# Optimization experiments

Hardware: AMD Instinct MI355X
Metric: run time of the kernel (lower is better)

The kernel has to match this reference:

```python
import jax, jax.numpy as jnp
import numpy as np

D_MODEL = 1024; D_STATE = 128; HEADDIM = 64; D_CONV = 4; CHUNK = 256
D_INNER = 2 * D_MODEL; NHEADS = D_INNER // HEADDIM
CONV_DIM = D_INNER + 2 * D_STATE
D_IN_PROJ = 2 * D_INNER + 2 * D_STATE + NHEADS
POOL_SIZE = 50; SUMMARY_DIM = 64; TAU1 = 0.5; TAU2 = 0.3
RET_HEAD_DIM = SUMMARY_DIM // 4  # CrossTokenRetrieval n_heads=4
SCORER_HID = int(D_MODEL * 0.25)
B_SZ = 2; T_LEN = 1024
EPS = 1e-5


def _rmsnorm(x, w):
    var = jnp.mean(jnp.square(x), axis=-1, keepdims=True)
    return x * jax.lax.rsqrt(var + EPS) * w


def _ssd(xd, dA, Bm, Cm):
    # Mamba2 SSD chunked scan. xd=(b,T,h,p)=x*dt, dA=(b,T,h)=dt*A, Bm/Cm=(b,T,n)
    b, T, h, p = xd.shape
    c = T // CHUNK; l = CHUNK
    xd = xd.reshape(b, c, l, h, p)
    dA = dA.reshape(b, c, l, h).transpose(0, 3, 1, 2)           # (b,h,c,l)
    Bm = Bm.reshape(b, c, l, -1); Cm = Cm.reshape(b, c, l, -1)  # (b,c,l,n)
    cs = jnp.cumsum(dA, axis=-1)                                # (b,h,c,l)
    mask = jnp.tril(jnp.ones((l, l), bool))
    seg = jnp.where(mask, cs[..., :, None] - cs[..., None, :], -jnp.inf)
    L = jnp.exp(seg)                                            # (b,h,c,l,s)
    y_diag = jnp.einsum('bcln,bcsn,bhcls,bcshp->bclhp', Cm, Bm, L, xd)
    decay_states = jnp.exp(cs[..., -1:] - cs)                   # (b,h,c,l)
    states = jnp.einsum('bcln,bhcl,bclhp->bchpn', Bm, decay_states, xd)
    chunk_sum = jnp.pad(cs[..., -1], ((0, 0), (0, 0), (1, 0)))  # (b,h,c+1)
    cs2 = jnp.cumsum(chunk_sum, axis=-1)
    maskc = jnp.tril(jnp.ones((c + 1, c + 1), bool))
    segc = jnp.where(maskc, cs2[..., :, None] - cs2[..., None, :], -jnp.inf)
    decay_chunk = jnp.exp(segc)                                 # (b,h,c+1,c+1)
    states = jnp.concatenate([jnp.zeros_like(states[:, :1]), states], axis=1)
    prev = jnp.einsum('bhzc,bchpn->bzhpn', decay_chunk, states)[:, :-1]
    y_off = jnp.einsum('bcln,bchpn,bhcl->bclhp', Cm, prev, jnp.exp(cs))
    return (y_diag + y_off).reshape(b, T, h, p)


def _forward(x, norm_w, in_proj_w, conv_w, conv_b, dt_bias, A_log, D, ssm_norm_w,
             out_proj_w, scorer_w1, scorer_w2, summ_w, q_w, k_w, v_w, gate_w):
    b, T, _ = x.shape
    residual = x
    xn = _rmsnorm(x, norm_w)
    # --- Mamba2 ---
    zxbcdt = xn @ in_proj_w                                     # (b,T,4384)
    z = zxbcdt[..., :D_INNER]
    xBC = zxbcdt[..., D_INNER:D_INNER + CONV_DIM]
    dt = jax.nn.softplus(zxbcdt[..., -NHEADS:] + dt_bias)       # (b,T,h)
    xpad = jnp.pad(xBC, ((0, 0), (D_CONV - 1, 0), (0, 0)))      # causal depthwise conv
    conv = conv_b + sum(xpad[:, k:k + T, :] * conv_w[:, k] for k in range(D_CONV))
    xBC = jax.nn.silu(conv)
    xs = xBC[..., :D_INNER].reshape(b, T, NHEADS, HEADDIM)
    Bm = xBC[..., D_INNER:D_INNER + D_STATE]
    Cm = xBC[..., D_INNER + D_STATE:]
    A = -jnp.exp(A_log)                                         # (h,)
    y = _ssd(xs * dt[..., None], dt * A, Bm, Cm)
    y = y + xs * D[None, None, :, None]
    y = y.reshape(b, T, D_INNER)
    y = _rmsnorm(y * jax.nn.silu(z), ssm_norm_w)                # gated RMSNorm
    y = y @ out_proj_w                                          # (b,T,d_model)
    # --- token importance scorer ---
    scores = jax.nn.sigmoid(jax.nn.relu(y @ scorer_w1) @ scorer_w2)[..., 0]  # (b,T)
    # --- memory pool update (layer_idx % freq == 0) ---
    summaries = (y @ summ_w).reshape(-1, SUMMARY_DIM)
    flat_scores = scores.reshape(-1)

    def step(carry, inp):
        pool, prios, count = carry
        s, sc = inp
        valid = sc > TAU1
        not_full = count < POOL_SIZE
        min_idx = jnp.argmin(prios)
        idx = jnp.where(not_full, count, min_idx)
        write = valid & (not_full | (sc > prios[min_idx]))
        pool = pool.at[idx].set(jnp.where(write, s, pool[idx]))
        prios = prios.at[idx].set(jnp.where(write, sc, prios[idx]))
        count = count + (valid & not_full).astype(jnp.int32)
        return (pool, prios, count), None

    init = (jnp.zeros((POOL_SIZE, SUMMARY_DIM), y.dtype),
            jnp.zeros((POOL_SIZE,), y.dtype), jnp.int32(0))
    (pool, prios, count), _ = jax.lax.scan(step, init, (summaries, flat_scores))
    # --- retrieval + gated fusion ---
    q = y @ q_w                                                 # (b,T,S)
    kk = pool @ k_w                                             # (P,S)
    vv = pool @ v_w                                             # (P,d_model)
    logits = jnp.einsum('bts,ps->btp', q, kk) / (RET_HEAD_DIM ** 0.5)
    valid_slot = jnp.arange(POOL_SIZE) < count
    logits = jnp.where(valid_slot, logits, -1e9)
    retrieved = jnp.einsum('btp,pd->btd', jax.nn.softmax(logits, axis=-1), vv)
    gate = jax.nn.sigmoid(jnp.concatenate([y, retrieved], axis=-1) @ gate_w)
    cond = (jnp.mean(scores) > TAU2) & (count > 0)
    y = jnp.where(cond, y + gate * retrieved, y)
    return residual + y


def setup_inputs() -> dict:
    key = jax.random.key(0)
    ks = jax.random.split(key, 16)
    w = lambda k, shape, s=0.02: jax.random.normal(k, shape, jnp.float32) * s
    dt = jax.random.uniform(ks[5], (NHEADS,), jnp.float32, 0.001, 0.1)
    return {
        'x': jax.random.normal(ks[0], (B_SZ, T_LEN, D_MODEL), jnp.float32),
        'norm_w': jnp.ones((D_MODEL,), jnp.float32),
        'in_proj_w': w(ks[1], (D_MODEL, D_IN_PROJ)),
        'conv_w': w(ks[2], (CONV_DIM, D_CONV), 0.1),
        'conv_b': jnp.zeros((CONV_DIM,), jnp.float32),
        'dt_bias': jnp.log(jnp.expm1(dt)),
        'A_log': jnp.log(jax.random.uniform(ks[6], (NHEADS,), jnp.float32, 1.0, 16.0)),
        'D': jnp.ones((NHEADS,), jnp.float32),
        'ssm_norm_w': jnp.ones((D_INNER,), jnp.float32),
        'out_proj_w': w(ks[7], (D_INNER, D_MODEL)),
        'scorer_w1': w(ks[8], (D_MODEL, SCORER_HID)),
        'scorer_w2': w(ks[9], (SCORER_HID, 1), 0.2),
        'summ_w': w(ks[10], (D_MODEL, SUMMARY_DIM)),
        'q_w': w(ks[11], (D_MODEL, SUMMARY_DIM)),
        'k_w': w(ks[12], (SUMMARY_DIM, SUMMARY_DIM)),
        'v_w': w(ks[13], (SUMMARY_DIM, D_MODEL)),
        'gate_w': w(ks[14], (2 * D_MODEL, D_MODEL)),
    }


def reference(x, norm_w, in_proj_w, conv_w, conv_b, dt_bias, A_log, D, ssm_norm_w,
              out_proj_w, scorer_w1, scorer_w2, summ_w, q_w, k_w, v_w, gate_w):
    return _forward(x, norm_w, in_proj_w, conv_w, conv_b, dt_bias, A_log, D, ssm_norm_w,
                    out_proj_w, scorer_w1, scorer_w2, summ_w, q_w, k_w, v_w, gate_w)
```

## Files before the change

kernel.cpp:

```cpp
#include <hip/hip_runtime.h>
#include <math.h>

#define NHEADS 32
#define D_INNER 2048
#define CONV_DIM 2304
#define D_IN_PROJ 4384
#define POOL_N 50
#define BT 2048

typedef __attribute__((ext_vector_type(8))) short short8;
typedef __attribute__((ext_vector_type(4))) float f32x4;

__device__ __forceinline__ float sigmoidf_(float x){ return 1.f/(1.f+expf(-x)); }
__device__ __forceinline__ ushort f2bf(float f){
  union{float f; unsigned u;} v; v.f=f;
  unsigned r = v.u + 0x7fffu + ((v.u>>16)&1u);
  return (ushort)(r>>16);
}
__device__ __forceinline__ void gload16(const void* g, void* l){
  __builtin_amdgcn_global_load_lds(
    (const __attribute__((address_space(1))) unsigned int*)g,
    (__attribute__((address_space(3))) unsigned int*)l, 16, 0, 0);
}

__global__ __launch_bounds__(256) void k_rmsnorm_x(const float* __restrict__ x, const float* __restrict__ w, ushort* __restrict__ xn){
  int r = blockIdx.x;
  const float* xr = x + (size_t)r*1024;
  float v[4]; float ss=0.f;
  for(int i=0;i<4;i++){ v[i]=xr[threadIdx.x+i*256]; ss+=v[i]*v[i]; }
  __shared__ float red[4];
  for(int off=32;off;off>>=1) ss += __shfl_down(ss,off,64);
  int wid=threadIdx.x>>6, lane=threadIdx.x&63;
  if(lane==0) red[wid]=ss;
  __syncthreads();
  float tot=red[0]+red[1]+red[2]+red[3];
  float rs=rsqrtf(tot*(1.f/1024.f)+1e-5f);
  for(int i=0;i<4;i++){ int c=threadIdx.x+i*256; xn[(size_t)r*1024+c]=f2bf(v[i]*rs*w[c]); }
}

__global__ __launch_bounds__(256) void k_transpose_cvt(const float* __restrict__ src, ushort* __restrict__ dst, int R, int C){
  __shared__ float tile[32][33];
  int c0 = blockIdx.x*32, r0 = blockIdx.y*32;
  int tx = threadIdx.x&31, ty = threadIdx.x>>5;
  for(int i=0;i<4;i++){ int r = r0+ty+i*8; tile[ty+i*8][tx] = src[(size_t)r*C + c0+tx]; }
  __syncthreads();
  for(int i=0;i<4;i++){ int c = c0+ty+i*8; dst[(size_t)c*R + r0+tx] = f2bf(tile[tx][ty+i*8]); }
}

__global__ __launch_bounds__(256) void gemm_bf16(const ushort* __restrict__ A, const ushort* __restrict__ Bt,
    float* __restrict__ C, ushort* __restrict__ Cb, int M, int N, int K, int act, int nbx){
  __shared__ __align__(16) ushort As[2][128*64];
  __shared__ __align__(16) ushort Bs[2][128*64];
  int wg = blockIdx.x, nwg = gridDim.x;
  if((nwg & 7)==0){ int cpx = nwg>>3; wg = (wg&7)*cpx + (wg>>3); }
  int bx = wg % nbx, by = wg / nbx;
  int n0 = bx*128, m0 = by*128;
  int tid = threadIdx.x;
  int lane = tid&63, w = tid>>6;
  int wr = (w>>1)*64, wc = (w&1)*64;
  f32x4 acc[4][4];
  for(int i=0;i<4;i++)for(int j=0;j<4;j++)acc[i][j]=(f32x4){0.f,0.f,0.f,0.f};
  int col16s = (tid&7) ^ ((tid>>3)&7);
  int r0t = tid>>3;
  const char* AG[4]; const char* BG[4];
  #pragma unroll
  for(int c=0;c<4;c++){
    int r = r0t + c*32;
    AG[c] = (const char*)(A + (size_t)(m0+r)*K + col16s*8);
    int br = n0 + r;
    BG[c] = (const char*)(Bt + (size_t)((br<N)?br:0)*K + col16s*8);
  }
  int nk = K >> 6;
  int fr = lane&15, fq = lane>>4;
  {
    #pragma unroll
    for(int c=0;c<4;c++){
      gload16(AG[c], (char*)As[0] + (c*256 + w*64)*16);
      gload16(BG[c], (char*)Bs[0] + (c*256 + w*64)*16);
    }
  }
  for(int ks=0; ks<nk; ks++){
    int cur = ks&1;
    if(ks+1 < nk){
      size_t kb = (size_t)(ks+1)*128;
      #pragma unroll
      for(int c=0;c<4;c++){
        gload16(AG[c]+kb, (char*)As[cur^1] + (c*256 + w*64)*16);
        gload16(BG[c]+kb, (char*)Bs[cur^1] + (c*256 + w*64)*16);
      }
      asm volatile("s_waitcnt vmcnt(8)" ::: "memory");
    } else {
      asm volatile("s_waitcnt vmcnt(0)" ::: "memory");
    }
    __builtin_amdgcn_s_barrier();
    __builtin_amdgcn_sched_barrier(0);
    #pragma unroll
    for(int kk=0;kk<2;kk++){
      short8 af[4], bfr[4];
      #pragma unroll
      for(int i=0;i<4;i++){
        int rl = wr+i*16+fr;
        int off = ((rl<<7) + (kk<<6) + (fq<<4)) ^ ((rl&7)<<4);
        af[i] = *(const short8*)((char*)As[cur] + off);
      }
      #pragma unroll
      for(int j=0;j<4;j++){
        int rl = wc+j*16+fr;
        int off = ((rl<<7) + (kk<<6) + (fq<<4)) ^ ((rl&7)<<4);
        bfr[j] = *(const short8*)((char*)Bs[cur] + off);
      }
      #pragma unroll
      for(int i=0;i<4;i++)
        #pragma unroll
        for(int j=0;j<4;j++)
          acc[i][j] = __builtin_amdgcn_mfma_f32_16x16x32_bf16(af[i], bfr[j], acc[i][j], 0,0,0);
    }
    asm volatile("s_waitcnt lgkmcnt(0)" ::: "memory");
    __builtin_amdgcn_sched_barrier(0);
    __builtin_amdgcn_s_barrier();
  }
  int rbase = m0 + wr + fq*4;
  for(int i=0;i<4;i++){
    for(int j=0;j<4;j++){
      int col = n0 + wc + j*16 + fr;
      if(col < N){
        for(int r=0;r<4;r++){
          float v = acc[i][j][r];
          if(act) v = fmaxf(v,0.f);
          size_t idx = (size_t)(rbase + i*16 + r)*N + col;
          C[idx] = v;
          if(Cb) Cb[idx] = f2bf(v);
        }
      }
    }
  }
}

__global__ void k_dt(const float* __restrict__ zxb, const float* __restrict__ dt_bias, float* __restrict__ dtb){
  int o = blockIdx.x*256+threadIdx.x;
  int r = o>>5, h = o&31;
  float v = zxb[(size_t)r*D_IN_PROJ + 4352 + h] + dt_bias[h];
  dtb[o] = (v>20.f) ? v : log1pf(expf(v));
}

__global__ void k_conv4(const float* __restrict__ zxb, const float* __restrict__ cw, const float* __restrict__ cb, float* __restrict__ xbc){
  int o = blockIdx.x*256+threadIdx.x;
  if(o >= 2048*576) return;
  int ch4 = (o % 576)*4; int rt = o / 576;
  int b = rt>>10, t = rt&1023;
  float a[4];
  { float4 cbv = *(const float4*)(cb + ch4); a[0]=cbv.x; a[1]=cbv.y; a[2]=cbv.z; a[3]=cbv.w; }
  float cwa[4][4];
  for(int c2=0;c2<4;c2++){
    float4 v = *(const float4*)(cw + (ch4+c2)*4);
    cwa[c2][0]=v.x; cwa[c2][1]=v.y; cwa[c2][2]=v.z; cwa[c2][3]=v.w;
  }
  for(int k=0;k<4;k++){
    int tt = t-3+k;
    if(tt>=0){
      float4 v = *(const float4*)(zxb + (size_t)(b*1024+tt)*D_IN_PROJ + 2048 + ch4);
      a[0] += v.x*cwa[0][k]; a[1] += v.y*cwa[1][k];
      a[2] += v.z*cwa[2][k]; a[3] += v.w*cwa[3][k];
    }
  }
  float4 o4;
  o4.x = a[0]*sigmoidf_(a[0]); o4.y = a[1]*sigmoidf_(a[1]);
  o4.z = a[2]*sigmoidf_(a[2]); o4.w = a[3]*sigmoidf_(a[3]);
  *(float4*)(xbc + (size_t)rt*CONV_DIM + ch4) = o4;
}

__global__ __launch_bounds__(256) void k_gt(const float* __restrict__ xbc, float* __restrict__ Gt){
  int bc = blockIdx.x >> 8;
  int tile = blockIdx.x & 255;
  int l0 = (tile>>4)<<4, s0 = (tile&15)<<4;
  int b = bc>>2, c = bc&3;
  int row0 = b*1024 + c*256;
  __shared__ float Cs[16][130], Bs2[16][130];
  int tid = threadIdx.x;
  for(int i=0;i<8;i++){ int e=tid+i*256; int rr=e>>7, n=e&127;
    Cs[rr][n]  = xbc[(size_t)(row0+l0+rr)*CONV_DIM + 2176 + n];
    Bs2[rr][n] = xbc[(size_t)(row0+s0+rr)*CONV_DIM + 2048 + n];
  }
  __syncthreads();
  int tx = tid&15, ty = tid>>4;
  float acc=0.f;
  for(int n=0;n<128;n++) acc += Cs[tx][n]*Bs2[ty][n];
  Gt[(size_t)bc*65536 + (size_t)(s0+ty)*256 + (l0+tx)] = acc;
}

__global__ __launch_bounds__(512) void k_ssd1w(const float* __restrict__ xbc, const float* __restrict__ dtb,
    const float* __restrict__ A_log, const float* __restrict__ Gt,
    float* __restrict__ ybuf, float* __restrict__ states, float* __restrict__ csb, float* __restrict__ sdA){
  int blk = blockIdx.x;
  int bc = blk>>5, h = blk&31;
  int b = bc>>2, c = bc&3;
  int row0 = b*1024 + c*256;
  int tid = threadIdx.x;
  __shared__ float cs[256];
  __shared__ float dts[256];
  __shared__ float dec[256];
  __shared__ __align__(16) ushort xdT[64*256];
  __shared__ __align__(16) ushort Mw[4*64*32];
  __shared__ __align__(16) ushort Bw[4*32*256];
  float Ah = -expf(A_log[h]);
  if(tid < 256){
    float dtv = dtb[(size_t)(row0+tid)*32 + h];
    dts[tid] = dtv;
    cs[tid] = dtv*Ah;
  }
  __syncthreads();
  for(int o=1;o<256;o<<=1){
    float add = 0.f;
    if(tid<256 && tid>=o) add = cs[tid-o];
    __syncthreads();
    if(tid<256) cs[tid] += add;
    __syncthreads();
  }
  float cslast = cs[255];
  if(tid < 256){
    float csl = cs[tid];
    csb[blk*256+tid] = csl;
    dec[tid] = expf(cslast - csl);
    if(tid==0) sdA[blk] = cslast;
  }
  {
    int p = tid&63, g = tid>>6;
    for(int i=0;i<32;i++){
      int l = g + 8*i;
      float v = xbc[(size_t)(row0+l)*CONV_DIM + h*64 + p] * dts[l];
      int off = ((p<<9) + (l<<1)) ^ ((p&7)<<4);
      *(ushort*)((char*)xdT + off) = f2bf(v);
    }
  }
  __syncthreads();

  int w = tid>>6, lane = tid&63;
  int fr = lane&15, fq = lane>>4;
  const float* gt = Gt + (size_t)bc*65536;
  if(w < 4){
    int rowl = w*64 + lane;
    float csl_w = cs[rowl];
    f32x4 accY[4][4];
    for(int i=0;i<4;i++)for(int j=0;j<4;j++)accY[i][j]=(f32x4){0.f,0.f,0.f,0.f};
    int nk = 2*(w+1);
    for(int ks=0; ks<nk; ks++){
      int s0 = ks*32;
      float cs_s0 = cs[s0];
      float ev = expf(cs_s0 - cs[s0 + (lane&31)]);
      float el = expf(csl_w - cs_s0);
      for(int j=0;j<4;j++){
        short8 mp;
        for(int k=0;k<8;k++){
          int s2 = j*8+k;
          int s = s0 + s2;
          float gv = gt[(size_t)s*256 + rowl];
          float esv = __shfl(ev, s2, 64);
          float m = (s <= rowl) ? gv*el*esv : 0.f;
          mp[k] = (short)f2bf(m);
        }
        int off = (w<<12) + ((((lane)<<6) + (j<<4)) ^ ((lane&7)<<4));
        *(short8*)((char*)Mw + off) = mp;
      }
      asm volatile("s_waitcnt lgkmcnt(0)" ::: "memory");
      __builtin_amdgcn_sched_barrier(0);
      short8 af[4], bv4[4];
      for(int i=0;i<4;i++){
        int lp = i*16 + fr;
        int off = (w<<12) + (((lp<<6) + (fq<<4)) ^ ((lp&7)<<4));
        af[i] = *(const short8*)((char*)Mw + off);
      }
      for(int j=0;j<4;j++){
        int p = j*16 + fr;
        int off = ((p<<9) + ((s0 + fq*8)<<1)) ^ ((p&7)<<4);
        bv4[j] = *(const short8*)((char*)xdT + off);
      }
      for(int i=0;i<4;i++)
        for(int j=0;j<4;j++)
          accY[i][j] = __builtin_amdgcn_mfma_f32_16x16x32_bf16(af[i], bv4[j], accY[i][j], 0,0,0);
      asm volatile("" ::: "memory");
    }
    for(int i=0;i<4;i++){
      int l = 64*w + i*16 + fq*4;
      for(int j=0;j<4;j++){
        int p = j*16 + fr;
        for(int r=0;r<4;r++)
          ybuf[(size_t)(row0+l+r)*2048 + h*64 + p] = accY[i][j][r];
      }
    }
  } else {
    int sw = w-4, nbase = sw*32;
    {
      int nn = lane&31, half = lane>>5;
      for(int i=0;i<128;i++){
        int l = half + 2*i;
        float v = xbc[(size_t)(row0+l)*CONV_DIM + 2048 + nbase + nn] * dec[l];
        int off = (sw<<14) + (((nn<<9) + (l<<1)) ^ ((nn&7)<<4));
        *(ushort*)((char*)Bw + off) = f2bf(v);
      }
    }
    asm volatile("s_waitcnt lgkmcnt(0)" ::: "memory");
    __builtin_amdgcn_sched_barrier(0);
    f32x4 accS[4][2];
    for(int i=0;i<4;i++)for(int j=0;j<2;j++)accS[i][j]=(f32x4){0.f,0.f,0.f,0.f};
    for(int ks=0;ks<8;ks++){
      int l0 = ks*32;
      short8 aS[4], bS[2];
      for(int i=0;i<4;i++){
        int p = i*16 + fr;
        int off = ((p<<9) + ((l0+fq*8)<<1)) ^ ((p&7)<<4);
        aS[i] = *(const short8*)((char*)xdT + off);
      }
      for(int j=0;j<2;j++){
        int nn = j*16 + fr;
        int off = (sw<<14) + (((nn<<9) + ((l0+fq*8)<<1)) ^ ((nn&7)<<4));
        bS[j] = *(const short8*)((char*)Bw + off);
      }
      for(int i=0;i<4;i++)
        for(int j=0;j<2;j++)
          accS[i][j] = __builtin_amdgcn_mfma_f32_16x16x32_bf16(aS[i], bS[j], accS[i][j], 0,0,0);
    }
    for(int i=0;i<4;i++){
      int p = i*16 + fq*4;
      for(int j=0;j<2;j++){
        int n = nbase + j*16 + fr;
        for(int r=0;r<4;r++)
          states[(size_t)blk*8192 + (size_t)(p+r)*128 + n] = accS[i][j][r];
      }
    }
  }
}

__global__ __launch_bounds__(256) void k_ssd2(const float* __restrict__ states, const float* __restrict__ sdA, float* __restrict__ prevb){
  int idx = blockIdx.x*256 + threadIdx.x;
  int e = idx & 8191;
  int h = (idx >> 13) & 31;
  int b = idx >> 18;
  float run = 0.f;
  for(int c=0;c<4;c++){
    int sblk = (b*4+c)*32 + h;
    size_t base = (size_t)sblk*8192 + e;
    prevb[base] = run;
    run = (run + states[base]) * expf(sdA[sblk]);
  }
}

__global__ __launch_bounds__(256) void k_ssd3m(const float* __restrict__ xbc, const float* __restrict__ csb,
    const float* __restrict__ prevb, const float* __restrict__ Dp, float* __restrict__ ybuf){
  int blk = blockIdx.x; int bc = blk>>5, h = blk&31; int b=bc>>2, c=bc&3;
  int row0 = b*1024+c*256;
  int tid = threadIdx.x;
  __shared__ __align__(16) ushort Cs[256*128];
  __shared__ __align__(16) ushort Ps[64*128];
  __shared__ float cse[256];
  for(int i=0;i<128;i++){
    int id = tid + i*256;
    int n = id & 127, l = id >> 7;
    float v = xbc[(size_t)(row0+l)*CONV_DIM + 2176 + n];
    int off = ((l<<8) + (n<<1)) ^ ((l&7)<<4);
    *(ushort*)((char*)Cs + off) = f2bf(v);
  }
  for(int i=0;i<32;i++){
    int id = tid + i*256;
    int n = id & 127, p = id >> 7;
    float v = prevb[(size_t)blk*8192 + id];
    int off = ((p<<8) + (n<<1)) ^ ((p&7)<<4);
    *(ushort*)((char*)Ps + off) = f2bf(v);
  }
  cse[tid] = expf(csb[blk*256+tid]);
  __syncthreads();
  int w=tid>>6, lane=tid&63, fr=lane&15, fq=lane>>4;
  f32x4 acc[4][4];
  for(int i=0;i<4;i++)for(int j=0;j<4;j++)acc[i][j]=(f32x4){0.f,0.f,0.f,0.f};
  for(int ks=0;ks<4;ks++){
    int n0 = ks*32;
    short8 af[4], bf_[4];
    for(int i=0;i<4;i++){
      int l = w*64 + i*16 + fr;
      int off = ((l<<8) + ((n0+fq*8)<<1)) ^ ((l&7)<<4);
      af[i] = *(const short8*)((char*)Cs + off);
    }
    for(int j=0;j<4;j++){
      int p = j*16 + fr;
      int off = ((p<<8) + ((n0+fq*8)<<1)) ^ ((p&7)<<4);
      bf_[j] = *(const short8*)((char*)Ps + off);
    }
    for(int i=0;i<4;i++)
      for(int j=0;j<4;j++)
        acc[i][j] = __builtin_amdgcn_mfma_f32_16x16x32_bf16(af[i], bf_[j], acc[i][j], 0,0,0);
  }
  float Dh = Dp[h];
  for(int i=0;i<4;i++){
    int lbase = 64*w + i*16 + fq*4;
    for(int r=0;r<4;r++){
      int l = lbase + r;
      float e = cse[l];
      size_t rowoff = (size_t)(row0+l)*CONV_DIM + h*64;
      size_t yb = (size_t)(row0+l)*2048 + h*64;
      for(int j=0;j<4;j++){
        int p = j*16 + fr;
        float xs = xbc[rowoff + p];
        ybuf[yb+p] += e*acc[i][j][r] + xs*Dh;
      }
    }
  }
}

__global__ __launch_bounds__(256) void k_gate_norm(const float* __restrict__ y, const float* __restrict__ zxb,
    const float* __restrict__ w, ushort* __restrict__ yb16){
  int r = blockIdx.x;
  const float* zr = zxb + (size_t)r*D_IN_PROJ;
  const float* yr = y + (size_t)r*2048;
  float v[8]; float ss=0.f;
  for(int i=0;i<8;i++){ int c=threadIdx.x+i*256; float z=zr[c]; float g=yr[c]*(z*sigmoidf_(z)); v[i]=g; ss+=g*g; }
  __shared__ float red[4];
  for(int off=32;off;off>>=1) ss += __shfl_down(ss,off,64);
  int wid=threadIdx.x>>6, lane=threadIdx.x&63;
  if(lane==0) red[wid]=ss;
  __syncthreads();
  float tot=red[0]+red[1]+red[2]+red[3];
  float rs=rsqrtf(tot*(1.f/2048.f)+1e-5f);
  for(int i=0;i<8;i++){ int c=threadIdx.x+i*256; yb16[(size_t)r*2048+c]=f2bf(v[i]*rs*w[c]); }
}

__global__ void k_scorer2(const float* __restrict__ h1, const float* __restrict__ w2, float* __restrict__ scores){
  int r = blockIdx.x; int lane = threadIdx.x;
  float s=0.f;
  for(int k=0;k<4;k++){ int c=lane+k*64; s += h1[(size_t)r*256+c]*w2[c]; }
  for(int off=32;off;off>>=1) s += __shfl_down(s,off,64);
  if(lane==0) scores[r]=sigmoidf_(s);
}

__global__ void k_pool(const float* __restrict__ scores,
                       int* __restrict__ countws, int* __restrict__ winners, float* __restrict__ condf){
  __shared__ float scs[BT];
  int lane = threadIdx.x;
  float own[32];
  float ssum = 0.f; int vcnt = 0;
  #pragma unroll
  for(int i=0;i<32;i++){
    float s0 = scores[i*64 + lane];
    own[i] = s0; scs[i*64+lane] = s0;
    ssum += s0; vcnt += (s0 > 0.5f) ? 1 : 0;
  }
  float ts = ssum; int tv = vcnt;
  for(int off=32;off;off>>=1){ ts += __shfl_xor(ts,off,64); tv += __shfl_xor(tv,off,64); }
  int count = tv < POOL_N ? tv : POOL_N;
  bool fallback = false;
  if(tv <= POOL_N){
    int base = 0;
    #pragma unroll
    for(int i=0;i<32;i++){
      bool sel = own[i] > 0.5f;
      unsigned long long mask = __ballot(sel);
      int pre = __popcll(mask & ((1ull<<lane)-1ull));
      if(sel) winners[base + pre] = i*64 + lane;
      base += __popcll(mask);
    }
    for(int r=base+lane; r<POOL_N; r+=64) winners[r] = -1;
  } else {
    unsigned lo = 0u, hi = 0x3F800000u;
    while(hi - lo > 1u){
      unsigned mid = (lo + hi) >> 1;
      float midf = __uint_as_float(mid);
      int cnt = 0;
      #pragma unroll
      for(int i=0;i<32;i++) cnt += (own[i] >= midf) ? 1 : 0;
      for(int off=32;off;off>>=1) cnt += __shfl_xor(cnt,off,64);
      if(cnt >= POOL_N) lo = mid; else hi = mid;
    }
    float v50 = __uint_as_float(lo);
    int cl = 0;
    #pragma unroll
    for(int i=0;i<32;i++) cl += (own[i] >= v50) ? 1 : 0;
    for(int off=32;off;off>>=1) cl += __shfl_xor(cl,off,64);
    if(cl == POOL_N){
      int base = 0;
      #pragma unroll
      for(int i=0;i<32;i++){
        bool sel = own[i] >= v50;
        unsigned long long mask = __ballot(sel);
        int pre = __popcll(mask & ((1ull<<lane)-1ull));
        if(sel) winners[base + pre] = i*64 + lane;
        base += __popcll(mask);
      }
    } else fallback = true;
  }
  if(fallback){
    float prio = 0.f; int winner = -1; int cnt2 = 0;
    float curmin = 0.f; int curargmin = 0;
    for(int b0=0;b0<BT;b0+=64){
      float ow = scs[b0+lane];
      unsigned long long mask = (cnt2 < POOL_N) ? __ballot(ow > 0.5f) : __ballot(ow > curmin);
      while(mask){
        int j = __ffsll(mask) - 1;
        mask &= mask - 1ull;
        float sc = __shfl(ow, j, 64);
        if(cnt2 < POOL_N){
          if(lane == cnt2){ prio = sc; winner = b0+j; }
          cnt2++;
          if(cnt2 == POOL_N){
            float v = (lane < POOL_N)? prio : INFINITY; int idx = lane;
            for(int off=32;off;off>>=1){
              float ov = __shfl_xor(v,off,64); int oi = __shfl_xor(idx,off,64);
              if(ov < v || (ov==v && oi<idx)){ v=ov; idx=oi; }
            }
            curmin = v; curargmin = idx;
          }
        } else if(sc > curmin){
          if(lane == curargmin){ prio = sc; winner = b0+j; }
          float v = (lane < POOL_N)? prio : INFINITY; int idx = lane;
          for(int off=32;off;off>>=1){
            float ov = __shfl_xor(v,off,64); int oi = __shfl_xor(idx,off,64);
            if(ov < v || (ov==v && oi<idx)){ v=ov; idx=oi; }
          }
          curmin = v; curargmin = idx;
        }
      }
    }
    if(lane < POOL_N) winners[lane] = winner;
  }
  if(lane==0){
    countws[0] = count;
    float mean = ts*(1.f/2048.f);
    condf[0] = (mean>0.3f && count>0)? 1.f : 0.f;
  }
}

__global__ void k_poolg(const float* __restrict__ sq, const int* __restrict__ winners, float* __restrict__ poolb){
  int p = blockIdx.x; int lane = threadIdx.x;
  int wi = winners[p];
  poolb[p*64+lane] = (wi>=0)? sq[(size_t)wi*128+lane] : 0.f;
}

__global__ void k_kk(const float* __restrict__ pool, const float* __restrict__ k_w, float* __restrict__ kkT){
  int o = blockIdx.x*256+threadIdx.x;
  if(o >= 64*POOL_N) return;
  int j = o/POOL_N, p = o%POOL_N;
  float s=0.f;
  for(int k=0;k<64;k++) s += pool[p*64+k]*k_w[k*64+j];
  kkT[j*64+p]=s;
}

__global__ void k_vvT(const float* __restrict__ pool, const float* __restrict__ v_w, ushort* __restrict__ vvT){
  int o = blockIdx.x*256+threadIdx.x;
  if(o >= 1024*64) return;
  int d = o>>6, p = o&63;
  float s=0.f;
  if(p < POOL_N)
    for(int k=0;k<64;k++) s += pool[p*64+k]*v_w[(size_t)k*1024+d];
  vvT[o] = f2bf(s);
}

__global__ __launch_bounds__(256) void k_probs(const float* __restrict__ sq, const float* __restrict__ kkT,
    const int* __restrict__ counti, ushort* __restrict__ Pb){
  __shared__ float qs[4][64];
  int tid = threadIdx.x;
  int w = tid>>6, lane = tid&63;
  int r = blockIdx.x*4 + w;
  qs[w][lane] = sq[(size_t)r*128 + 64 + lane];
  __syncthreads();
  int count = counti[0];
  float logit = -1e9f;
  if(lane < POOL_N && lane < count){
    float s=0.f;
    for(int k=0;k<64;k++) s += qs[w][k]*kkT[k*64+lane];
    logit = s*0.25f;
  }
  float m = logit;
  for(int off=32;off;off>>=1) m = fmaxf(m, __shfl_xor(m,off,64));
  float e = expf(logit-m);
  float sum = e;
  for(int off=32;off;off>>=1) sum += __shfl_xor(sum,off,64);
  Pb[(size_t)r*64 + lane] = f2bf(e/sum);
}

__global__ __launch_bounds__(256) void k_pv(const ushort* __restrict__ Pb, const ushort* __restrict__ vvT,
    float* __restrict__ retr){
  __shared__ __align__(16) ushort As[128*64];
  __shared__ __align__(16) ushort Bs[128*64];
  int m0 = (blockIdx.x >> 3)*128, n0 = (blockIdx.x & 7)*128;
  int tid = threadIdx.x;
  int row = tid>>1, half = tid&1;
  {
    const uint4* sa = (const uint4*)(Pb  + (size_t)(m0+row)*64 + half*32);
    const uint4* sb = (const uint4*)(vvT + (size_t)(n0+row)*64 + half*32);
    for(int ch=0;ch<4;ch++){
      int boff = (row<<7) + (half<<6) + (ch<<4);
      int so = boff ^ ((row&7)<<4);
      *(uint4*)((char*)As + so) = sa[ch];
      *(uint4*)((char*)Bs + so) = sb[ch];
    }
  }
  __syncthreads();
  int w=tid>>6, lane=tid&63, fr=lane&15, fq=lane>>4;
  int wr=(w>>1)*64, wc=(w&1)*64;
  f32x4 acc[4][4];
  for(int i=0;i<4;i++)for(int j=0;j<4;j++)acc[i][j]=(f32x4){0.f,0.f,0.f,0.f};
  for(int k0=0;k0<64;k0+=32){
    short8 af[4], bf_[4];
    for(int i=0;i<4;i++){
      int r = wr+i*16+fr;
      int boff = ((r<<7) + ((k0+fq*8)<<1)) ^ ((r&7)<<4);
      af[i] = *(const short8*)((char*)As + boff);
    }
    for(int j=0;j<4;j++){
      int r = wc+j*16+fr;
      int boff = ((r<<7) + ((k0+fq*8)<<1)) ^ ((r&7)<<4);
      bf_[j] = *(const short8*)((char*)Bs + boff);
    }
    for(int i=0;i<4;i++)
      for(int j=0;j<4;j++)
        acc[i][j] = __builtin_amdgcn_mfma_f32_16x16x32_bf16(af[i], bf_[j], acc[i][j], 0,0,0);
  }
  int rbase = m0 + wr + fq*4;
  for(int i=0;i<4;i++){
    for(int j=0;j<4;j++){
      int col = n0 + wc + j*16 + fr;
      for(int r=0;r<4;r++)
        retr[(size_t)(rbase + i*16 + r)*1024 + col] = acc[i][j][r];
    }
  }
}

__global__ void k_concat(const float* __restrict__ yout, const float* __restrict__ retr, ushort* __restrict__ cc){
  int o = blockIdx.x*256+threadIdx.x;
  int r = o>>11, c2 = o&2047;
  cc[o] = f2bf((c2<1024)? yout[(size_t)r*1024+c2] : retr[(size_t)r*1024+(c2-1024)]);
}

__global__ void k_final(const float* __restrict__ x, const float* __restrict__ yout, const float* __restrict__ g,
   const float* __restrict__ retr, const float* __restrict__ condf, float* __restrict__ out){
  int o = blockIdx.x*256+threadIdx.x;
  float gv = sigmoidf_(g[o]);
  out[o] = x[o] + yout[o] + condf[0]*gv*retr[o];
}

static inline void gemmb(hipStream_t s, const ushort*A,const ushort*Bt,float*C,ushort*Cb,int M,int N,int K,int act){
  int nbx = (N+127)/128;
  int nwg = nbx * (M/128);
  hipLaunchKernelGGL(gemm_bf16,dim3(nwg),dim3(256),0,s,A,Bt,C,Cb,M,N,K,act,nbx);
}

extern "C" void kernel_launch(void* const* d_in, const int* in_sizes, int n_in,
                              void* d_out, int out_size, void* d_ws, size_t ws_size,
                              hipStream_t stream) {
  const float* x        = (const float*)d_in[0];
  const float* norm_w   = (const float*)d_in[1];
  const float* in_proj_w= (const float*)d_in[2];
  const float* conv_w   = (const float*)d_in[3];
  const float* conv_b   = (const float*)d_in[4];
  const float* dt_bias  = (const float*)d_in[5];
  const float* A_log    = (const float*)d_in[6];
  const float* Dp       = (const float*)d_in[7];
  const float* ssm_norm_w=(const float*)d_in[8];
  const float* out_proj_w=(const float*)d_in[9];
  const float* scorer_w1= (const float*)d_in[10];
  const float* scorer_w2= (const float*)d_in[11];
  const float* summ_w   = (const float*)d_in[12];
  const float* q_w      = (const float*)d_in[13];
  const float* k_w      = (const float*)d_in[14];
  const float* v_w      = (const float*)d_in[15];
  const float* gate_w   = (const float*)d_in[16];
  float* out = (float*)d_out;

  unsigned char* base = (unsigned char*)d_ws;
  size_t off = 0;
  auto FB = [&](size_t bytes)->void*{ void* p = base+off; off = (off+bytes+255)&~(size_t)255; return p; };
  float* zxb   = (float*)FB((size_t)2048*D_IN_PROJ*4);
  float* dtb   = (float*)FB((size_t)2048*32*4);
  float* xbc   = (float*)FB((size_t)2048*CONV_DIM*4);
  float* csb   = (float*)FB((size_t)256*256*4);
  float* sdA   = (float*)FB(1024);
  float* states= (float*)FB((size_t)256*8192*4);
  float* prevb = (float*)FB((size_t)256*8192*4);
  float* ybuf  = (float*)FB((size_t)2048*2048*4);
  float* yout  = (float*)FB((size_t)2048*1024*4);
  float* scores= (float*)FB(2048*4);
  float* summ  = (float*)FB((size_t)2048*64*4);
  float* qb    = (float*)FB((size_t)2048*64*4);
  float* poolb = (float*)FB(POOL_N*64*4);
  float* prios = (float*)FB(256);
  float* miscf = (float*)FB(256);
  int*   counti= (int*)FB(256);
  int*   winners=(int*)FB(256);
  unsigned char* RX = (unsigned char*)FB((size_t)4194304);
  unsigned char* W1 = (unsigned char*)FB((size_t)8978432);

  ushort* xnb   = (ushort*)RX;
  ushort* sqT   = (ushort*)RX;
  ushort* summT = (ushort*)RX;
  ushort* qT    = (ushort*)(RX + 131072);
  float*  h1    = (float*) (RX + 262144);
  float*  kkT   = (float*) (RX + 2359296);
  ushort* vvT   = (ushort*)(RX + 2375680);
  ushort* Pb    = (ushort*)(RX + 2506752);
  ushort* inT   = (ushort*)W1;
  ushort* outT  = (ushort*)W1;
  ushort* gateT = (ushort*)(W1 + 4194304);
  ushort* sc1T  = (ushort*)(W1 + 8388608);
  float*  Gt    = yout;
  ushort* ybf   = (ushort*)prevb;
  float*  gbuf  = prevb;
  float*  retr  = states;
  ushort* ccb   = (ushort*)ybuf;
  ushort* youtb = (ushort*)((unsigned char*)ybuf + 8388608);
  float*  sq    = summ;
  (void)qb; (void)prios;

  hipLaunchKernelGGL(k_transpose_cvt, dim3(137,32), dim3(256), 0, stream, in_proj_w, inT, 1024, 4384);
  k_rmsnorm_x<<<2048,256,0,stream>>>(x, norm_w, xnb);
  gemmb(stream, xnb, inT, zxb, nullptr, 2048, D_IN_PROJ, 1024, 0);
  hipLaunchKernelGGL(k_transpose_cvt, dim3(32,64), dim3(256), 0, stream, out_proj_w, outT, 2048, 1024);
  hipLaunchKernelGGL(k_transpose_cvt, dim3(32,64), dim3(256), 0, stream, gate_w, gateT, 2048, 1024);
  hipLaunchKernelGGL(k_transpose_cvt, dim3(8,32), dim3(256), 0, stream, scorer_w1, sc1T, 1024, 256);
  hipLaunchKernelGGL(k_transpose_cvt, dim3(2,32), dim3(256), 0, stream, summ_w, summT, 1024, 64);
  hipLaunchKernelGGL(k_transpose_cvt, dim3(2,32), dim3(256), 0, stream, q_w, qT, 1024, 64);
  k_dt<<<256,256,0,stream>>>(zxb, dt_bias, dtb);
  k_conv4<<<4608,256,0,stream>>>(zxb, conv_w, conv_b, xbc);
  k_gt<<<2048,256,0,stream>>>(xbc, Gt);
  k_ssd1w<<<256,512,0,stream>>>(xbc, dtb, A_log, Gt, ybuf, states, csb, sdA);
  k_ssd2<<<2048,256,0,stream>>>(states, sdA, prevb);
  k_ssd3m<<<256,256,0,stream>>>(xbc, csb, prevb, Dp, ybuf);
  k_gate_norm<<<2048,256,0,stream>>>(ybuf, zxb, ssm_norm_w, ybf);
  gemmb(stream, ybf, outT, yout, youtb, 2048, 1024, 2048, 0);
  gemmb(stream, youtb, sc1T, h1, nullptr, 2048, 256, 1024, 1);
  k_scorer2<<<2048,64,0,stream>>>(h1, scorer_w2, scores);
  gemmb(stream, youtb, sqT, sq, nullptr, 2048, 128, 1024, 0);
  k_pool<<<1,64,0,stream>>>(scores, counti, winners, miscf);
  k_poolg<<<POOL_N,64,0,stream>>>(sq, winners, poolb);
  k_kk<<<(64*POOL_N+255)/256,256,0,stream>>>(poolb, k_w, kkT);
  k_vvT<<<256,256,0,stream>>>(poolb, v_w, vvT);
  k_probs<<<512,256,0,stream>>>(sq, kkT, counti, Pb);
  k_pv<<<128,256,0,stream>>>(Pb, vvT, retr);
  k_concat<<<16384,256,0,stream>>>(yout, retr, ccb);
  gemmb(stream, ccb, gateT, gbuf, nullptr, 2048, 1024, 2048, 0);
  k_final<<<8192,256,0,stream>>>(x, yout, gbuf, retr, miscf, out);
  (void)in_sizes; (void)n_in; (void)out_size; (void)ws_size;
}
```

Before: 323.5 us.

## Fuse scorer/summary GEMMs, drop concat, and fuse gate GEMM with final epilogue

The scorer-hidden, summary and query projections are merged into one GEMM with N=384, with the ReLU moved into the scorer reduction. The concat kernel is removed: the new gate GEMM reads its K range from the bf16 y_out buffer for the first half and from a bf16 retrieval buffer written by k_pv for the second half. The final residual, sigmoid gate and conditional mix are computed in that GEMM's epilogue. This cuts several launches and full-size intermediate round trips. The cost is buffer aliasing changes and a gate GEMM launched as only 128 workgroups.

```diff
diff --git a/kernel.cpp b/kernel.cpp
--- a/kernel.cpp
+++ b/kernel.cpp
@@ -131,6 +131,97 @@
           C[idx] = v;
           if(Cb) Cb[idx] = f2bf(v);
         }
+      }
+    }
+  }
+}
+
+__global__ __launch_bounds__(256) void gemm_gate(const ushort* __restrict__ Ay, const ushort* __restrict__ Ar,
+    const ushort* __restrict__ Bt, const float* __restrict__ x, const float* __restrict__ yout,
+    const float* __restrict__ retr, const float* __restrict__ condf, float* __restrict__ out){
+  __shared__ __align__(16) ushort As[2][128*64];
+  __shared__ __align__(16) ushort Bs[2][128*64];
+  const int nbx = 8, N = 1024;
+  int wg = blockIdx.x, nwg = gridDim.x;
+  if((nwg & 7)==0){ int cpx = nwg>>3; wg = (wg&7)*cpx + (wg>>3); }
+  int bx = wg % nbx, by = wg / nbx;
+  int n0 = bx*128, m0 = by*128;
+  int tid = threadIdx.x;
+  int lane = tid&63, w = tid>>6;
+  int wr = (w>>1)*64, wc = (w&1)*64;
+  f32x4 acc[4][4];
+  for(int i=0;i<4;i++)for(int j=0;j<4;j++)acc[i][j]=(f32x4){0.f,0.f,0.f,0.f};
+  int col16s = (tid&7) ^ ((tid>>3)&7);
+  int r0t = tid>>3;
+  const char* AGy[4]; const char* AGr[4]; const char* BG[4];
+  #pragma unroll
+  for(int c=0;c<4;c++){
+    int r = r0t + c*32;
+    AGy[c] = (const char*)(Ay + (size_t)(m0+r)*1024 + col16s*8);
+    AGr[c] = (const char*)(Ar + (size_t)(m0+r)*1024 + col16s*8);
+    BG[c]  = (const char*)(Bt + (size_t)(n0+r)*2048 + col16s*8);
+  }
+  const int nk = 32;
+  int fr = lane&15, fq = lane>>4;
+  {
+    #pragma unroll
+    for(int c=0;c<4;c++){
+      gload16(AGy[c], (char*)As[0] + (c*256 + w*64)*16);
+      gload16(BG[c],  (char*)Bs[0] + (c*256 + w*64)*16);
+    }
+  }
+  for(int ks=0; ks<nk; ks++){
+    int cur = ks&1;
+    if(ks+1 < nk){
+      int t = ks+1;
+      size_t kbA = (size_t)((t<16)? t : t-16)*128;
+      size_t kbB = (size_t)t*128;
+      #pragma unroll
+      for(int c=0;c<4;c++){
+        const char* asrc = (t<16) ? (AGy[c]+kbA) : (AGr[c]+kbA);
+        gload16(asrc, (char*)As[cur^1] + (c*256 + w*64)*16);
+        gload16(BG[c]+kbB, (char*)Bs[cur^1] + (c*256 + w*64)*16);
+      }
+      asm volatile("s_waitcnt vmcnt(8)" ::: "memory");
+    } else {
+      asm volatile("s_waitcnt vmcnt(0)" ::: "memory");
+    }
+    __builtin_amdgcn_s_barrier();
+    __builtin_amdgcn_sched_barrier(0);
+    #pragma unroll
+    for(int kk=0;kk<2;kk++){
+      short8 af[4], bfr[4];
+      #pragma unroll
+      for(int i=0;i<4;i++){
+        int rl = wr+i*16+fr;
+        int off = ((rl<<7) + (kk<<6) + (fq<<4)) ^ ((rl&7)<<4);
+        af[i] = *(const short8*)((char*)As[cur] + off);
+      }
+      #pragma unroll
+      for(int j=0;j<4;j++){
+        int rl = wc+j*16+fr;
+        int off = ((rl<<7) + (kk<<6) + (fq<<4)) ^ ((rl&7)<<4);
+        bfr[j] = *(const short8*)((char*)Bs[cur] + off);
+      }
+      #pragma unroll
+      for(int i=0;i<4;i++)
+        #pragma unroll
+        for(int j=0;j<4;j++)
+          acc[i][j] = __builtin_amdgcn_mfma_f32_16x16x32_bf16(af[i], bfr[j], acc[i][j], 0,0,0);
+    }
+    asm volatile("s_waitcnt lgkmcnt(0)" ::: "memory");
+    __builtin_amdgcn_sched_barrier(0);
+    __builtin_amdgcn_s_barrier();
+  }
+  float cond = condf[0];
+  int rbase = m0 + wr + fq*4;
+  for(int i=0;i<4;i++){
+    for(int j=0;j<4;j++){
+      int col = n0 + wc + j*16 + fr;
+      for(int r=0;r<4;r++){
+        size_t idx = (size_t)(rbase + i*16 + r)*1024 + col;
+        float gv = sigmoidf_(acc[i][j][r]);
+        out[idx] = x[idx] + yout[idx] + cond*gv*retr[idx];
       }
     }
   }
@@ -425,7 +516,7 @@
 __global__ void k_scorer2(const float* __restrict__ h1, const float* __restrict__ w2, float* __restrict__ scores){
   int r = blockIdx.x; int lane = threadIdx.x;
   float s=0.f;
-  for(int k=0;k<4;k++){ int c=lane+k*64; s += h1[(size_t)r*256+c]*w2[c]; }
+  for(int k=0;k<4;k++){ int c=lane+k*64; s += fmaxf(h1[(size_t)r*384+c],0.f)*w2[c]; }
   for(int off=32;off;off>>=1) s += __shfl_down(s,off,64);
   if(lane==0) scores[r]=sigmoidf_(s);
 }
@@ -526,10 +617,10 @@
   }
 }
 
-__global__ void k_poolg(const float* __restrict__ sq, const int* __restrict__ winners, float* __restrict__ poolb){
+__global__ void k_poolg(const float* __restrict__ hsq, const int* __restrict__ winners, float* __restrict__ poolb){
   int p = blockIdx.x; int lane = threadIdx.x;
   int wi = winners[p];
-  poolb[p*64+lane] = (wi>=0)? sq[(size_t)wi*128+lane] : 0.f;
+  poolb[p*64+lane] = (wi>=0)? hsq[(size_t)wi*384 + 256 + lane] : 0.f;
 }
 
 __global__ void k_kk(const float* __restrict__ pool, const float* __restrict__ k_w, float* __restrict__ kkT){
@@ -551,13 +642,13 @@
   vvT[o] = f2bf(s);
 }
 
-__global__ __launch_bounds__(256) void k_probs(const float* __restrict__ sq, const float* __restrict__ kkT,
+__global__ __launch_bounds__(256) void k_probs(const float* __restrict__ hsq, const float* __restrict__ kkT,
     const int* __restrict__ counti, ushort* __restrict__ Pb){
   __shared__ float qs[4][64];
   int tid = threadIdx.x;
   int w = tid>>6, lane = tid&63;
   int r = blockIdx.x*4 + w;
-  qs[w][lane] = sq[(size_t)r*128 + 64 + lane];
+  qs[w][lane] = hsq[(size_t)r*384 + 320 + lane];
   __syncthreads();
   int count = counti[0];
   float logit = -1e9f;
@@ -575,7 +666,7 @@
 }
 
 __global__ __launch_bounds__(256) void k_pv(const ushort* __restrict__ Pb, const ushort* __restrict__ vvT,
-    float* __restrict__ retr){
+    float* __restrict__ retr, ushort* __restrict__ retrb){
   __shared__ __align__(16) ushort As[128*64];
   __shared__ __align__(16) ushort Bs[128*64];
   int m0 = (blockIdx.x >> 3)*128, n0 = (blockIdx.x & 7)*128;
@@ -616,23 +707,14 @@
   for(int i=0;i<4;i++){
     for(int j=0;j<4;j++){
       int col = n0 + wc + j*16 + fr;
-      for(int r=0;r<4;r++)
-        retr[(size_t)(rbase + i*16 + r)*1024 + col] = acc[i][j][r];
-    }
-  }
-}
-
-__global__ void k_concat(const float* __restrict__ yout, const float* __restrict__ retr, ushort* __restrict__ cc){
-  int o = blockIdx.x*256+threadIdx.x;
-  int r = o>>11, c2 = o&2047;
-  cc[o] = f2bf((c2<1024)? yout[(size_t)r*1024+c2] : retr[(size_t)r*1024+(c2-1024)]);
-}
-
-__global__ void k_final(const float* __restrict__ x, const float* __restrict__ yout, const float* __restrict__ g,
-   const float* __restrict__ retr, const float* __restrict__ condf, float* __restrict__ out){
-  int o = blockIdx.x*256+threadIdx.x;
-  float gv = sigmoidf_(g[o]);
-  out[o] = x[o] + yout[o] + condf[0]*gv*retr[o];
+      for(int r=0;r<4;r++){
+        float v = acc[i][j][r];
+        size_t idx = (size_t)(rbase + i*16 + r)*1024 + col;
+        retr[idx] = v;
+        retrb[idx] = f2bf(v);
+      }
+    }
+  }
 }
 
 static inline void gemmb(hipStream_t s, const ushort*A,const ushort*Bt,float*C,ushort*Cb,int M,int N,int K,int act){
@@ -687,34 +769,29 @@
   unsigned char* W1 = (unsigned char*)FB((size_t)8978432);
 
   ushort* xnb   = (ushort*)RX;
-  ushort* sqT   = (ushort*)RX;
-  ushort* summT = (ushort*)RX;
-  ushort* qT    = (ushort*)(RX + 131072);
-  float*  h1    = (float*) (RX + 262144);
-  float*  kkT   = (float*) (RX + 2359296);
-  ushort* vvT   = (ushort*)(RX + 2375680);
-  ushort* Pb    = (ushort*)(RX + 2506752);
+  ushort* scsqT = (ushort*)RX;
+  float*  hsq   = (float*) (RX + 786432);
+  float*  kkT   = (float*) ((unsigned char*)qb + 262144);
+  ushort* vvT   = (ushort*)summ;
+  ushort* Pb    = (ushort*)qb;
   ushort* inT   = (ushort*)W1;
   ushort* outT  = (ushort*)W1;
   ushort* gateT = (ushort*)(W1 + 4194304);
-  ushort* sc1T  = (ushort*)(W1 + 8388608);
   float*  Gt    = yout;
   ushort* ybf   = (ushort*)prevb;
-  float*  gbuf  = prevb;
   float*  retr  = states;
-  ushort* ccb   = (ushort*)ybuf;
+  ushort* retrb = (ushort*)ybuf;
   ushort* youtb = (ushort*)((unsigned char*)ybuf + 8388608);
-  float*  sq    = summ;
-  (void)qb; (void)prios;
+  (void)prios;
 
   hipLaunchKernelGGL(k_transpose_cvt, dim3(137,32), dim3(256), 0, stream, in_proj_w, inT, 1024, 4384);
   k_rmsnorm_x<<<2048,256,0,stream>>>(x, norm_w, xnb);
   gemmb(stream, xnb, inT, zxb, nullptr, 2048, D_IN_PROJ, 1024, 0);
   hipLaunchKernelGGL(k_transpose_cvt, dim3(32,64), dim3(256), 0, stream, out_proj_w, outT, 2048, 1024);
   hipLaunchKernelGGL(k_transpose_cvt, dim3(32,64), dim3(256), 0, stream, gate_w, gateT, 2048, 1024);
-  hipLaunchKernelGGL(k_transpose_cvt, dim3(8,32), dim3(256), 0, stream, scorer_w1, sc1T, 1024, 256);
-  hipLaunchKernelGGL(k_transpose_cvt, dim3(2,32), dim3(256), 0, stream, summ_w, summT, 1024, 64);
-  hipLaunchKernelGGL(k_transpose_cvt, dim3(2,32), dim3(256), 0, stream, q_w, qT, 1024, 64);
+  hipLaunchKernelGGL(k_transpose_cvt, dim3(8,32), dim3(256), 0, stream, scorer_w1, scsqT, 1024, 256);
+  hipLaunchKernelGGL(k_transpose_cvt, dim3(2,32), dim3(256), 0, stream, summ_w, scsqT + 256*1024, 1024, 64);
+  hipLaunchKernelGGL(k_transpose_cvt, dim3(2,32), dim3(256), 0, stream, q_w, scsqT + 320*1024, 1024, 64);
   k_dt<<<256,256,0,stream>>>(zxb, dt_bias, dtb);
   k_conv4<<<4608,256,0,stream>>>(zxb, conv_w, conv_b, xbc);
   k_gt<<<2048,256,0,stream>>>(xbc, Gt);
@@ -723,17 +800,15 @@
   k_ssd3m<<<256,256,0,stream>>>(xbc, csb, prevb, Dp, ybuf);
   k_gate_norm<<<2048,256,0,stream>>>(ybuf, zxb, ssm_norm_w, ybf);
   gemmb(stream, ybf, outT, yout, youtb, 2048, 1024, 2048, 0);
-  gemmb(stream, youtb, sc1T, h1, nullptr, 2048, 256, 1024, 1);
-  k_scorer2<<<2048,64,0,stream>>>(h1, scorer_w2, scores);
-  gemmb(stream, youtb, sqT, sq, nullptr, 2048, 128, 1024, 0);
+  gemmb(stream, youtb, scsqT, hsq, nullptr, 2048, 384, 1024, 0);
+  k_scorer2<<<2048,64,0,stream>>>(hsq, scorer_w2, scores);
   k_pool<<<1,64,0,stream>>>(scores, counti, winners, miscf);
-  k_poolg<<<POOL_N,64,0,stream>>>(sq, winners, poolb);
+  k_poolg<<<POOL_N,64,0,stream>>>(hsq, winners, poolb);
   k_kk<<<(64*POOL_N+255)/256,256,0,stream>>>(poolb, k_w, kkT);
   k_vvT<<<256,256,0,stream>>>(poolb, v_w, vvT);
-  k_probs<<<512,256,0,stream>>>(sq, kkT, counti, Pb);
-  k_pv<<<128,256,0,stream>>>(Pb, vvT, retr);
-  k_concat<<<16384,256,0,stream>>>(yout, retr, ccb);
-  gemmb(stream, ccb, gateT, gbuf, nullptr, 2048, 1024, 2048, 0);
-  k_final<<<8192,256,0,stream>>>(x, yout, gbuf, retr, miscf, out);
+  k_probs<<<512,256,0,stream>>>(hsq, kkT, counti, Pb);
+  k_pv<<<128,256,0,stream>>>(Pb, vvT, retr, retrb);
+  hipLaunchKernelGGL(gemm_gate, dim3(128), dim3(256), 0, stream,
+                     youtb, retrb, gateT, x, yout, retr, miscf, out);
   (void)in_sizes; (void)n_in; (void)out_size; (void)ws_size;
 }
```

Result: faster. 296.4 us (-8.4%).
